# Kernel tuning notes

Measured on AMD Instinct MI355X. Metric: run time of the kernel, lower is better.

## Reference

```python
import jax, jax.numpy as jnp
import numpy as np

P = 8192          # number of gaussians
H = 256           # image height
W = 256           # image width
TANX = 0.5        # tan(fovx/2)
TANY = 0.5        # tan(fovy/2)
SCALE_MOD = 1.0
CHUNK = 128       # gaussians composited per scan step
FX = W / (2.0 * TANX)   # focal_x, as in forward()
FY = H / (2.0 * TANY)   # focal_y


def setup_inputs() -> dict:
    key = jax.random.key(0)
    k = jax.random.split(key, 6)
    # place gaussians in the camera frustum (camera at origin, looking +z)
    z = jax.random.uniform(k[0], (P,), minval=2.0, maxval=6.0)
    xy = jax.random.normal(k[1], (P, 2)) * 0.4 * (z * TANX)[:, None]
    means3D = jnp.concatenate([xy, z[:, None]], axis=1)
    scales = 0.01 + 0.04 * jax.random.uniform(k[2], (P, 3))
    rotations = jax.random.normal(k[3], (P, 4))  # normalized inside reference
    opacities = 0.05 + 0.9 * jax.random.uniform(k[4], (P, 1))
    colors_precomp = jax.random.uniform(k[5], (P, 3))
    background = jnp.zeros((3,), jnp.float32)
    viewmatrix = jnp.eye(4, dtype=jnp.float32)  # row-vector convention: p' = [p,1] @ V
    znear, zfar = 0.01, 100.0
    Pm = np.zeros((4, 4), np.float32)
    Pm[0, 0] = 1.0 / TANX
    Pm[1, 1] = 1.0 / TANY
    Pm[2, 2] = zfar / (zfar - znear)
    Pm[2, 3] = -(zfar * znear) / (zfar - znear)
    Pm[3, 2] = 1.0
    projmatrix = jnp.asarray(Pm.T)  # row-vector convention (full proj = proj @ view, view = I)
    return dict(means3D=means3D, colors_precomp=colors_precomp, opacities=opacities,
                scales=scales, rotations=rotations, background=background,
                viewmatrix=viewmatrix, projmatrix=projmatrix)


def _quat_to_rot(q):
    q = q / jnp.linalg.norm(q, axis=-1, keepdims=True)
    r, x, y, z = q[:, 0], q[:, 1], q[:, 2], q[:, 3]
    R = jnp.stack([
        1 - 2 * (y * y + z * z), 2 * (x * y - r * z), 2 * (x * z + r * y),
        2 * (x * y + r * z), 1 - 2 * (x * x + z * z), 2 * (y * z - r * x),
        2 * (x * z - r * y), 2 * (y * z + r * x), 1 - 2 * (x * x + y * y)], axis=-1)
    return R.reshape(-1, 3, 3)


def _forward(means3D, colors_precomp, opacities, scales, rotations, background,
             viewmatrix, projmatrix):
    Pn = means3D.shape[0]
    # --- preprocess: 3D covariance from scale/rotation ---
    R = _quat_to_rot(rotations)
    s2 = (scales * SCALE_MOD) ** 2
    Sigma = jnp.einsum('pij,pj,pkj->pik', R, s2, R)  # R diag(s^2) R^T, [P,3,3]
    hom = jnp.concatenate([means3D, jnp.ones((Pn, 1), means3D.dtype)], axis=1)
    p_view = (hom @ viewmatrix)[:, :3]
    p_hom = hom @ projmatrix
    p_proj = p_hom[:, :3] / (p_hom[:, 3:4] + 1e-7)
    # NDC -> pixel centers
    mean2d = jnp.stack([((p_proj[:, 0] + 1.0) * W - 1.0) * 0.5,
                        ((p_proj[:, 1] + 1.0) * H - 1.0) * 0.5], axis=1)
    depths = p_view[:, 2]
    # --- EWA splatting: project covariance to 2D ---
    Rv = viewmatrix[:3, :3]
    cov_cam = jnp.einsum('ji,pjk,kl->pil', Rv, Sigma, Rv)  # Rv^T Sigma Rv
    tz = p_view[:, 2]
    tx = jnp.clip(p_view[:, 0] / tz, -1.3 * TANX, 1.3 * TANX) * tz
    ty = jnp.clip(p_view[:, 1] / tz, -1.3 * TANY, 1.3 * TANY) * tz
    zero = jnp.zeros_like(tz)
    J = jnp.stack([jnp.stack([FX / tz, zero, -FX * tx / tz ** 2], -1),
                   jnp.stack([zero, FY / tz, -FY * ty / tz ** 2], -1)], axis=1)  # [P,2,3]
    cov2d = jnp.einsum('pij,pjk,plk->pil', J, cov_cam, J)
    a = cov2d[:, 0, 0] + 0.3  # low-pass dilation as in 3DGS
    b = cov2d[:, 0, 1]
    c = cov2d[:, 1, 1] + 0.3
    det = a * c - b * b
    conic = jnp.stack([c, -b, a], axis=-1) / det[:, None]
    # --- global depth sort ---
    order = jnp.argsort(depths)
    m2d = mean2d[order]
    con = conic[order]
    col = colors_precomp[order]
    op = opacities[order]
    # --- per-pixel front-to-back alpha compositing ---
    px, py = jnp.meshgrid(jnp.arange(W, dtype=jnp.float32),
                          jnp.arange(H, dtype=jnp.float32))
    pixf = jnp.stack([px.ravel(), py.ravel()], axis=-1)  # [HW,2]
    n_chunks = Pn // CHUNK
    xs = (m2d.reshape(n_chunks, CHUNK, 2), con.reshape(n_chunks, CHUNK, 3),
          col.reshape(n_chunks, CHUNK, 3), op.reshape(n_chunks, CHUNK, 1))

    def step(carry, x):
        accum, T = carry
        m, cn, cl, o = x
        d = m[:, None, :] - pixf[None]  # [C,HW,2]
        power = (-0.5 * (cn[:, 0:1] * d[..., 0] ** 2 + cn[:, 2:3] * d[..., 1] ** 2)
                 - cn[:, 1:2] * d[..., 0] * d[..., 1])
        alpha = jnp.minimum(0.99, o * jnp.exp(power))
        alpha = jnp.where((power > 0.0) | (alpha < 1.0 / 255.0), 0.0, alpha)
        cp = jnp.cumprod(1.0 - alpha, axis=0)  # within-chunk transmittance
        excl = jnp.concatenate([jnp.ones((1, alpha.shape[1]), alpha.dtype), cp[:-1]], 0)
        wgt = alpha * excl * T[None]
        accum = accum + jnp.einsum('cp,cd->pd', wgt, cl)
        return (accum, T * cp[-1]), None

    accum0 = jnp.zeros((H * W, 3), jnp.float32)
    T0 = jnp.ones((H * W,), jnp.float32)
    (accum, T), _ = jax.lax.scan(step, (accum0, T0), xs)
    out = accum + T[:, None] * background[None]
    return out.reshape(H, W, 3).transpose(2, 0, 1)  # [3,H,W]


def reference(means3D, colors_precomp, opacities, scales, rotations, background,
              viewmatrix, projmatrix):
    return _forward(means3D, colors_precomp, opacities, scales, rotations,
                    background, viewmatrix, projmatrix)
```

## Files before the change

kernel.cpp:

```cpp
#include <hip/hip_runtime.h>


#define PN 8192
#define IH 256
#define IW 256


__global__ __launch_bounds__(256) void preprocess_kernel(
    const float* __restrict__ means, const float* __restrict__ colors,
    const float* __restrict__ ops, const float* __restrict__ scales,
    const float* __restrict__ rots, const float* __restrict__ V,
    const float* __restrict__ Pm, float* __restrict__ ws)
{
    int i = blockIdx.x * 256 + threadIdx.x;
    if (i >= PN) return;

    float mx3 = means[3 * i], my3 = means[3 * i + 1], mz3 = means[3 * i + 2];
    float qr = rots[4 * i], qx = rots[4 * i + 1], qy = rots[4 * i + 2], qz = rots[4 * i + 3];
    float qn = 1.0f / sqrtf(qr * qr + qx * qx + qy * qy + qz * qz);
    float r = qr * qn, x = qx * qn, y = qy * qn, z = qz * qn;

    float R00 = 1.f - 2.f * (y * y + z * z), R01 = 2.f * (x * y - r * z), R02 = 2.f * (x * z + r * y);
    float R10 = 2.f * (x * y + r * z), R11 = 1.f - 2.f * (x * x + z * z), R12 = 2.f * (y * z - r * x);
    float R20 = 2.f * (x * z - r * y), R21 = 2.f * (y * z + r * x), R22 = 1.f - 2.f * (x * x + y * y);

    float s0 = scales[3 * i];     s0 *= s0;
    float s1 = scales[3 * i + 1]; s1 *= s1;
    float s2 = scales[3 * i + 2]; s2 *= s2;

    float Sg[3][3];
    Sg[0][0] = R00 * R00 * s0 + R01 * R01 * s1 + R02 * R02 * s2;
    Sg[0][1] = R00 * R10 * s0 + R01 * R11 * s1 + R02 * R12 * s2;
    Sg[0][2] = R00 * R20 * s0 + R01 * R21 * s1 + R02 * R22 * s2;
    Sg[1][1] = R10 * R10 * s0 + R11 * R11 * s1 + R12 * R12 * s2;
    Sg[1][2] = R10 * R20 * s0 + R11 * R21 * s1 + R12 * R22 * s2;
    Sg[2][2] = R20 * R20 * s0 + R21 * R21 * s1 + R22 * R22 * s2;
    Sg[1][0] = Sg[0][1]; Sg[2][0] = Sg[0][2]; Sg[2][1] = Sg[1][2];

    float pv0 = mx3 * V[0] + my3 * V[4] + mz3 * V[8]  + V[12];
    float pv1 = mx3 * V[1] + my3 * V[5] + mz3 * V[9]  + V[13];
    float pv2 = mx3 * V[2] + my3 * V[6] + mz3 * V[10] + V[14];
    float ph0 = mx3 * Pm[0] + my3 * Pm[4] + mz3 * Pm[8]  + Pm[12];
    float ph1 = mx3 * Pm[1] + my3 * Pm[5] + mz3 * Pm[9]  + Pm[13];
    float ph3 = mx3 * Pm[3] + my3 * Pm[7] + mz3 * Pm[11] + Pm[15];
    float pw = 1.0f / (ph3 + 1e-7f);
    float m2x = ((ph0 * pw + 1.0f) * (float)IW - 1.0f) * 0.5f;
    float m2y = ((ph1 * pw + 1.0f) * (float)IH - 1.0f) * 0.5f;

    float Rv[3][3];
#pragma unroll
    for (int rr = 0; rr < 3; ++rr)
#pragma unroll
        for (int cc2 = 0; cc2 < 3; ++cc2) Rv[rr][cc2] = V[rr * 4 + cc2];
    float M[3][3];
#pragma unroll
    for (int j = 0; j < 3; ++j)
#pragma unroll
        for (int l = 0; l < 3; ++l)
            M[j][l] = Sg[j][0] * Rv[0][l] + Sg[j][1] * Rv[1][l] + Sg[j][2] * Rv[2][l];
    float cc[3][3];
#pragma unroll
    for (int ii = 0; ii < 3; ++ii)
#pragma unroll
        for (int l = 0; l < 3; ++l)
            cc[ii][l] = Rv[0][ii] * M[0][l] + Rv[1][ii] * M[1][l] + Rv[2][ii] * M[2][l];

    const float FX = 256.0f, FY = 256.0f;
    float tz = pv2;
    float itz = 1.0f / tz;
    float limx = 0.65f, limy = 0.65f;
    float txz = fminf(fmaxf(pv0 * itz, -limx), limx);
    float tyz = fminf(fmaxf(pv1 * itz, -limy), limy);
    float tx = txz * tz, ty = tyz * tz;
    float J00 = FX * itz, J02 = -FX * tx * itz * itz;
    float J11 = FY * itz, J12 = -FY * ty * itz * itz;

    float u00 = J00 * cc[0][0] + J02 * cc[2][0];
    float u01 = J00 * cc[0][1] + J02 * cc[2][1];
    float u02 = J00 * cc[0][2] + J02 * cc[2][2];
    float u11 = J11 * cc[1][1] + J12 * cc[2][1];
    float u12 = J11 * cc[1][2] + J12 * cc[2][2];
    float cov00 = u00 * J00 + u02 * J02;
    float cov01 = u01 * J11 + u02 * J12;
    float cov11 = u11 * J11 + u12 * J12;

    float a = cov00 + 0.3f;
    float b = cov01;
    float c = cov11 + 0.3f;
    float det = a * c - b * b;
    float idet = 1.0f / det;
    float cA = c * idet;
    float cB = -b * idet;
    float cC = a * idet;

    float ex = sqrtf(11.2f * a);
    float ey = sqrtf(11.2f * c);
    int x0 = max(0,  (int)floorf((m2x - ex) * 0.125f));
    int x1 = min(31, (int)floorf((m2x + ex) * 0.125f));
    int y0 = max(0,  (int)floorf((m2y - ey) * 0.125f));
    int y1 = min(31, (int)floorf((m2y + ey) * 0.125f));
    x0 = min(x0, 31); y0 = min(y0, 31); x1 = max(x1, 0); y1 = max(y1, 0);
    unsigned box = (unsigned)x0 | ((unsigned)x1 << 8) | ((unsigned)y0 << 16) | ((unsigned)y1 << 24);

    ws[i] = pv2;
    float4* preA = (float4*)(ws + PN);
    float4* preB = (float4*)(ws + 5 * PN);
    preA[i] = make_float4(m2x, m2y, cA, cB);
    preB[i] = make_float4(cC, ops[i], colors[3 * i], colors[3 * i + 1]);
    ws[9 * PN + i] = colors[3 * i + 2];
    ((unsigned*)(ws + 10 * PN))[i] = box;
}

__global__ __launch_bounds__(256) void sort_scatter_kernel(float* __restrict__ ws)
{
    const float* dep = ws;
    const float4* d4 = (const float4*)ws;
    int lane = threadIdx.x & 63;
    int wid = threadIdx.x >> 6;
    int gbase = blockIdx.x * 16 + wid * 4;

    float di0 = dep[gbase], di1 = dep[gbase + 1], di2 = dep[gbase + 2], di3 = dep[gbase + 3];
    int r0 = 0, r1 = 0, r2 = 0, r3 = 0;
#pragma unroll 4
    for (int k = 0; k < 32; ++k) {
        int j4 = k * 64 + lane;
        float4 d = d4[j4];
        int jb = j4 * 4;
        r0 += (d.x < di0) || (d.x == di0 && (jb    ) < gbase);
        r0 += (d.y < di0) || (d.y == di0 && (jb + 1) < gbase);
        r0 += (d.z < di0) || (d.z == di0 && (jb + 2) < gbase);
        r0 += (d.w < di0) || (d.w == di0 && (jb + 3) < gbase);
        r1 += (d.x < di1) || (d.x == di1 && (jb    ) < gbase + 1);
        r1 += (d.y < di1) || (d.y == di1 && (jb + 1) < gbase + 1);
        r1 += (d.z < di1) || (d.z == di1 && (jb + 2) < gbase + 1);
        r1 += (d.w < di1) || (d.w == di1 && (jb + 3) < gbase + 1);
        r2 += (d.x < di2) || (d.x == di2 && (jb    ) < gbase + 2);
        r2 += (d.y < di2) || (d.y == di2 && (jb + 1) < gbase + 2);
        r2 += (d.z < di2) || (d.z == di2 && (jb + 2) < gbase + 2);
        r2 += (d.w < di2) || (d.w == di2 && (jb + 3) < gbase + 2);
        r3 += (d.x < di3) || (d.x == di3 && (jb    ) < gbase + 3);
        r3 += (d.y < di3) || (d.y == di3 && (jb + 1) < gbase + 3);
        r3 += (d.z < di3) || (d.z == di3 && (jb + 2) < gbase + 3);
        r3 += (d.w < di3) || (d.w == di3 && (jb + 3) < gbase + 3);
    }
#pragma unroll
    for (int off = 1; off < 64; off <<= 1) {
        r0 += __shfl_xor(r0, off);
        r1 += __shfl_xor(r1, off);
        r2 += __shfl_xor(r2, off);
        r3 += __shfl_xor(r3, off);
    }
    if (lane < 4) {
        int rk = (lane == 0) ? r0 : (lane == 1) ? r1 : (lane == 2) ? r2 : r3;
        int i = gbase + lane;
        const float4* preA = (const float4*)(ws + PN);
        const float4* preB = (const float4*)(ws + 5 * PN);
        float4* sA = (float4*)(ws + 11 * PN);
        float4* sB = (float4*)(ws + 15 * PN);
        sA[rk] = preA[i];
        sB[rk] = preB[i];
        ws[19 * PN + rk] = ws[9 * PN + i];
        ((unsigned*)(ws + 20 * PN))[rk] = ((const unsigned*)(ws + 10 * PN))[i];
    }
}

__global__ __launch_bounds__(256) void raster_kernel(
    const float* __restrict__ ws, const float* __restrict__ bg,
    float* __restrict__ out)
{
    __shared__ float4 lsA[4][256];
    __shared__ float4 lsB[4][256];
    __shared__ float  seg[4][64 * 4];
    __shared__ float  lsb[4][256];
    volatile __shared__ float waveT[4];

    int tid = threadIdx.x;
    int lane = tid & 63, w = tid >> 6;
    int tileX = blockIdx.x & 31, tileY = blockIdx.x >> 5;
    int px = tileX * 8 + (lane & 7), py = tileY * 8 + (lane >> 3);
    float pxf = (float)px, pyf = (float)py;

    const float4* sA = (const float4*)(ws + 11 * PN);
    const float4* sB = (const float4*)(ws + 15 * PN);
    const float* sb = ws + 19 * PN;
    const unsigned* sbox = (const unsigned*)(ws + 20 * PN);

    if (tid < 4) waveT[tid] = 1.0f;
    __syncthreads();

    float T = 1.0f, ar = 0.0f, ag = 0.0f, ab = 0.0f;

    for (int chunk = w * 8; chunk < w * 8 + 8; ++chunk) {
        float pre = 1.0f;
        for (int q = 0; q < w; ++q) pre *= waveT[q];
        if (pre < 1e-4f) break;

        int base = chunk * 256;
        unsigned long long wv[4];
#pragma unroll
        for (int k = 0; k < 4; ++k) {
            unsigned bx = sbox[base + k * 64 + lane];
            bool ov = (tileX >= (int)(bx & 255)) & (tileX <= (int)((bx >> 8) & 255)) &
                      (tileY >= (int)((bx >> 16) & 255)) & (tileY <= (int)(bx >> 24));
            wv[k] = __ballot(ov);
        }
        if (!(wv[0] | wv[1] | wv[2] | wv[3])) continue;

        int cnt = 0;
#pragma unroll
        for (int k = 0; k < 4; ++k) {
            unsigned long long wk = wv[k];
            if ((wk >> lane) & 1ull) {
                int slot = cnt + (int)__popcll(wk & ((1ull << lane) - 1ull));
                int g = base + k * 64 + lane;
                lsA[w][slot] = sA[g];
                lsB[w][slot] = sB[g];
                lsb[w][slot] = sb[g];
            }
            cnt += (int)__popcll(wk);
        }
        asm volatile("s_waitcnt lgkmcnt(0)" ::: "memory");

        for (int j = 0; j < cnt; ++j) {
            float4 A = lsA[w][j];
            float4 B = lsB[w][j];
            float bcol = lsb[w][j];
            float dx = A.x - pxf, dy = A.y - pyf;
            float power = -0.5f * (A.z * dx * dx + B.x * dy * dy) - A.w * dx * dy;
            float alpha = fminf(0.99f, B.y * __expf(power));
            bool skip = (power > 0.0f) | (alpha < (1.0f / 255.0f));
            float a2 = skip ? 0.0f : alpha;
            float wgt = a2 * T;
            ar = fmaf(wgt, B.z, ar);
            ag = fmaf(wgt, B.w, ag);
            ab = fmaf(wgt, bcol, ab);
            T *= (1.0f - a2);
        }
        asm volatile("s_waitcnt lgkmcnt(0)" ::: "memory");

        if (__all(T < 1e-5f)) break;

        float tmax = T;
#pragma unroll
        for (int off = 1; off < 64; off <<= 1) tmax = fmaxf(tmax, __shfl_xor(tmax, off));
        if (lane == 0) waveT[w] = tmax;
    }

    seg[w][lane * 4 + 0] = ar;
    seg[w][lane * 4 + 1] = ag;
    seg[w][lane * 4 + 2] = ab;
    seg[w][lane * 4 + 3] = T;
    __syncthreads();

    if (w == 0) {
        float A0 = 0.f, A1 = 0.f, A2 = 0.f, Tt = 1.f;
#pragma unroll
        for (int q = 0; q < 4; ++q) {
            A0 += Tt * seg[q][lane * 4 + 0];
            A1 += Tt * seg[q][lane * 4 + 1];
            A2 += Tt * seg[q][lane * 4 + 2];
            Tt *= seg[q][lane * 4 + 3];
        }
        int pidx = py * IW + px;
        out[pidx]               = A0 + Tt * bg[0];
        out[IH * IW + pidx]     = A1 + Tt * bg[1];
        out[2 * IH * IW + pidx] = A2 + Tt * bg[2];
    }
}

extern "C" void kernel_launch(void* const* d_in, const int* in_sizes, int n_in,
                              void* d_out, int out_size, void* d_ws, size_t ws_size,
                              hipStream_t stream) {
    const float* means  = (const float*)d_in[0];
    const float* colors = (const float*)d_in[1];
    const float* ops    = (const float*)d_in[2];
    const float* scales = (const float*)d_in[3];
    const float* rots   = (const float*)d_in[4];
    const float* bg     = (const float*)d_in[5];
    const float* viewm  = (const float*)d_in[6];
    const float* projm  = (const float*)d_in[7];
    float* out = (float*)d_out;
    float* ws  = (float*)d_ws;

    hipLaunchKernelGGL(preprocess_kernel, dim3(PN / 256), dim3(256), 0, stream,
                       means, colors, ops, scales, rots, viewm, projm, ws);
    hipLaunchKernelGGL(sort_scatter_kernel, dim3(PN / 16), dim3(256), 0, stream, ws);
    hipLaunchKernelGGL(raster_kernel, dim3(1024), dim3(256), 0, stream, ws, bg, out);
}
```

Baseline: 112.1 us.

## Prefetch bbox words, scramble tile order, poll waveT mid-chunk, reuse shared buffer

The raster kernel now loads the next chunk's packed bounding boxes before processing the current chunk, so global load latency overlaps with compositing. Block-to-tile mapping is permuted with a multiply by 97 to spread heavy tiles across CUs. Waves other than wave 0 re-check the product of earlier waves' max transmittance every 16 gaussians and stop early once it falls below threshold. The final per-wave segment buffer now reuses lsb shared memory, which lowers LDS usage and may raise occupancy. The extra polling adds shared reads and branches inside the hot loop.

```diff
diff --git a/kernel.cpp b/kernel.cpp
--- a/kernel.cpp
+++ b/kernel.cpp
@@ -170,13 +170,13 @@
 {
     __shared__ float4 lsA[4][256];
     __shared__ float4 lsB[4][256];
-    __shared__ float  seg[4][64 * 4];
     __shared__ float  lsb[4][256];
     volatile __shared__ float waveT[4];
 
     int tid = threadIdx.x;
     int lane = tid & 63, w = tid >> 6;
-    int tileX = blockIdx.x & 31, tileY = blockIdx.x >> 5;
+    int tileIdx = (blockIdx.x * 97) & 1023;
+    int tileX = tileIdx & 31, tileY = tileIdx >> 5;
     int px = tileX * 8 + (lane & 7), py = tileY * 8 + (lane >> 3);
     float pxf = (float)px, pyf = (float)py;
 
@@ -190,22 +190,31 @@
 
     float T = 1.0f, ar = 0.0f, ag = 0.0f, ab = 0.0f;
 
-    for (int chunk = w * 8; chunk < w * 8 + 8; ++chunk) {
+    int c0 = w * 8;
+    unsigned bx[4];
+#pragma unroll
+    for (int k = 0; k < 4; ++k) bx[k] = sbox[c0 * 256 + k * 64 + lane];
+
+    bool dead = false;
+    for (int chunk = c0; chunk < c0 + 8 && !dead; ++chunk) {
         float pre = 1.0f;
         for (int q = 0; q < w; ++q) pre *= waveT[q];
         if (pre < 1e-4f) break;
 
+        unsigned long long wv[4];
+#pragma unroll
+        for (int k = 0; k < 4; ++k) {
+            bool ov = (tileX >= (int)(bx[k] & 255)) & (tileX <= (int)((bx[k] >> 8) & 255)) &
+                      (tileY >= (int)((bx[k] >> 16) & 255)) & (tileY <= (int)(bx[k] >> 24));
+            wv[k] = __ballot(ov);
+        }
+        if (chunk + 1 < c0 + 8) {
+#pragma unroll
+            for (int k = 0; k < 4; ++k) bx[k] = sbox[(chunk + 1) * 256 + k * 64 + lane];
+        }
+        if (!(wv[0] | wv[1] | wv[2] | wv[3])) continue;
+
         int base = chunk * 256;
-        unsigned long long wv[4];
-#pragma unroll
-        for (int k = 0; k < 4; ++k) {
-            unsigned bx = sbox[base + k * 64 + lane];
-            bool ov = (tileX >= (int)(bx & 255)) & (tileX <= (int)((bx >> 8) & 255)) &
-                      (tileY >= (int)((bx >> 16) & 255)) & (tileY <= (int)(bx >> 24));
-            wv[k] = __ballot(ov);
-        }
-        if (!(wv[0] | wv[1] | wv[2] | wv[3])) continue;
-
         int cnt = 0;
 #pragma unroll
         for (int k = 0; k < 4; ++k) {
@@ -222,6 +231,11 @@
         asm volatile("s_waitcnt lgkmcnt(0)" ::: "memory");
 
         for (int j = 0; j < cnt; ++j) {
+            if (w > 0 && (j & 15) == 15) {
+                float p2 = 1.0f;
+                for (int q = 0; q < w; ++q) p2 *= waveT[q];
+                if (p2 < 1e-4f) { dead = true; break; }
+            }
             float4 A = lsA[w][j];
             float4 B = lsB[w][j];
             float bcol = lsb[w][j];
@@ -246,20 +260,20 @@
         if (lane == 0) waveT[w] = tmax;
     }
 
-    seg[w][lane * 4 + 0] = ar;
-    seg[w][lane * 4 + 1] = ag;
-    seg[w][lane * 4 + 2] = ab;
-    seg[w][lane * 4 + 3] = T;
+    lsb[w][lane * 4 + 0] = ar;
+    lsb[w][lane * 4 + 1] = ag;
+    lsb[w][lane * 4 + 2] = ab;
+    lsb[w][lane * 4 + 3] = T;
     __syncthreads();
 
     if (w == 0) {
         float A0 = 0.f, A1 = 0.f, A2 = 0.f, Tt = 1.f;
 #pragma unroll
         for (int q = 0; q < 4; ++q) {
-            A0 += Tt * seg[q][lane * 4 + 0];
-            A1 += Tt * seg[q][lane * 4 + 1];
-            A2 += Tt * seg[q][lane * 4 + 2];
-            Tt *= seg[q][lane * 4 + 3];
+            A0 += Tt * lsb[q][lane * 4 + 0];
+            A1 += Tt * lsb[q][lane * 4 + 1];
+            A2 += Tt * lsb[q][lane * 4 + 2];
+            Tt *= lsb[q][lane * 4 + 3];
         }
         int pidx = py * IW + px;
         out[pidx]               = A0 + Tt * bg[0];
```

New measurement: 117.6 us. 1.05x slower.

## Unroll raster blend loop by two, reuse LDS buffer, swizzle tile order

Applied to the files above, without the earlier changes.

Unrolls the per-pixel compositing loop two gaussians at a time so the two exp and power evaluations can overlap, while the transmittance chain stays serial. Drops the separate seg shared array and reuses lsb for the cross-wave reduction, cutting LDS per block to help occupancy. Also XOR-swizzles block-to-tile mapping within each group of 256 blocks to spread heavy central tiles across CUs. The unroll may raise register pressure, and reusing lsb relies on the __syncthreads ordering after the loop.

```diff
diff --git a/kernel.cpp b/kernel.cpp
--- a/kernel.cpp
+++ b/kernel.cpp
@@ -170,13 +170,14 @@
 {
     __shared__ float4 lsA[4][256];
     __shared__ float4 lsB[4][256];
-    __shared__ float  seg[4][64 * 4];
     __shared__ float  lsb[4][256];
     volatile __shared__ float waveT[4];
 
     int tid = threadIdx.x;
     int lane = tid & 63, w = tid >> 6;
-    int tileX = blockIdx.x & 31, tileY = blockIdx.x >> 5;
+    int bq = blockIdx.x >> 8;
+    int tileIdx = (bq << 8) | ((blockIdx.x & 255) ^ ((bq * 9) & 31));
+    int tileX = tileIdx & 31, tileY = tileIdx >> 5;
     int px = tileX * 8 + (lane & 7), py = tileY * 8 + (lane >> 3);
     float pxf = (float)px, pyf = (float)py;
 
@@ -221,15 +222,35 @@
         }
         asm volatile("s_waitcnt lgkmcnt(0)" ::: "memory");
 
-        for (int j = 0; j < cnt; ++j) {
+        int j = 0;
+        for (; j + 1 < cnt; j += 2) {
+            float4 A0 = lsA[w][j],     B0 = lsB[w][j];
+            float4 A1 = lsA[w][j + 1], B1 = lsB[w][j + 1];
+            float b0 = lsb[w][j], b1 = lsb[w][j + 1];
+            float dx0 = A0.x - pxf, dy0 = A0.y - pyf;
+            float dx1 = A1.x - pxf, dy1 = A1.y - pyf;
+            float p0 = -0.5f * (A0.z * dx0 * dx0 + B0.x * dy0 * dy0) - A0.w * dx0 * dy0;
+            float p1 = -0.5f * (A1.z * dx1 * dx1 + B1.x * dy1 * dy1) - A1.w * dx1 * dy1;
+            float al0 = fminf(0.99f, B0.y * __expf(p0));
+            float al1 = fminf(0.99f, B1.y * __expf(p1));
+            float a0 = ((p0 > 0.0f) | (al0 < (1.0f / 255.0f))) ? 0.0f : al0;
+            float a1 = ((p1 > 0.0f) | (al1 < (1.0f / 255.0f))) ? 0.0f : al1;
+            float w0 = a0 * T;
+            float Tm = T * (1.0f - a0);
+            float w1 = a1 * Tm;
+            ar = fmaf(w0, B0.z, ar); ar = fmaf(w1, B1.z, ar);
+            ag = fmaf(w0, B0.w, ag); ag = fmaf(w1, B1.w, ag);
+            ab = fmaf(w0, b0, ab);   ab = fmaf(w1, b1, ab);
+            T = Tm * (1.0f - a1);
+        }
+        if (j < cnt) {
             float4 A = lsA[w][j];
             float4 B = lsB[w][j];
             float bcol = lsb[w][j];
             float dx = A.x - pxf, dy = A.y - pyf;
             float power = -0.5f * (A.z * dx * dx + B.x * dy * dy) - A.w * dx * dy;
             float alpha = fminf(0.99f, B.y * __expf(power));
-            bool skip = (power > 0.0f) | (alpha < (1.0f / 255.0f));
-            float a2 = skip ? 0.0f : alpha;
+            float a2 = ((power > 0.0f) | (alpha < (1.0f / 255.0f))) ? 0.0f : alpha;
             float wgt = a2 * T;
             ar = fmaf(wgt, B.z, ar);
             ag = fmaf(wgt, B.w, ag);
@@ -246,20 +267,20 @@
         if (lane == 0) waveT[w] = tmax;
     }
 
-    seg[w][lane * 4 + 0] = ar;
-    seg[w][lane * 4 + 1] = ag;
-    seg[w][lane * 4 + 2] = ab;
-    seg[w][lane * 4 + 3] = T;
+    lsb[w][lane * 4 + 0] = ar;
+    lsb[w][lane * 4 + 1] = ag;
+    lsb[w][lane * 4 + 2] = ab;
+    lsb[w][lane * 4 + 3] = T;
     __syncthreads();
 
     if (w == 0) {
         float A0 = 0.f, A1 = 0.f, A2 = 0.f, Tt = 1.f;
 #pragma unroll
         for (int q = 0; q < 4; ++q) {
-            A0 += Tt * seg[q][lane * 4 + 0];
-            A1 += Tt * seg[q][lane * 4 + 1];
-            A2 += Tt * seg[q][lane * 4 + 2];
-            Tt *= seg[q][lane * 4 + 3];
+            A0 += Tt * lsb[q][lane * 4 + 0];
+            A1 += Tt * lsb[q][lane * 4 + 1];
+            A2 += Tt * lsb[q][lane * 4 + 2];
+            Tt *= lsb[q][lane * 4 + 3];
         }
         int pidx = py * IW + px;
         out[pidx]               = A0 + Tt * bg[0];
```

After: 107.6 us. 4.0% less time.
